# Performance work log

Hardware: AMD Instinct MI355X
Metric: run time of the kernel (lower is better)

The kernel has to match this reference:

```python
import jax, jax.numpy as jnp
import numpy as np

SP = 4      # sp_size (number of simulated sequence-parallel ranks)
NH = 16     # num_attention_heads
HD = 64     # head_dim
HS = 1024   # hidden_size
B = 1       # batch
S = 8192    # global sequence length (SP chunks of 2048)


def setup_inputs() -> dict:
    key = jax.random.key(0)
    ks = jax.random.split(key, 9)
    w_scale = 1.0 / np.sqrt(HS)
    def w(k):
        # xavier-ish init, stored as [in, out] so y = x @ W + b
        return jax.random.uniform(k, (HS, HS), jnp.float32, -w_scale, w_scale)
    return {
        'hidden_states': jax.random.normal(ks[0], (B, S, HS), jnp.float32),
        'Wq': w(ks[1]), 'bq': jnp.zeros((HS,), jnp.float32),
        'Wk': w(ks[2]), 'bk': jnp.zeros((HS,), jnp.float32),
        'Wv': w(ks[3]), 'bv': jnp.zeros((HS,), jnp.float32),
        'Wo': w(ks[4]), 'bo': jnp.zeros((HS,), jnp.float32),
    }


def reference(hidden_states, Wq, bq, Wk, bk, Wv, bv, Wo, bo):
    b, s, _ = hidden_states.shape
    sc = s // SP  # per-rank chunk length
    inv_sqrt_hd = 1.0 / np.sqrt(HD)

    def heads(x):
        # [B, S, HS] -> [SP, B, NH, Sc, HD]
        return x.reshape(b, SP, sc, NH, HD).transpose(1, 0, 3, 2, 4)

    q = heads(hidden_states @ Wq + bq)
    k = heads(hidden_states @ Wk + bk)
    v = heads(hidden_states @ Wv + bv)

    out = jnp.zeros_like(q)
    # ring attention: at step i each rank r attends to chunk (r + i) mod SP
    for i in range(SP):
        ki = jnp.roll(k, -i, axis=0)
        vi = jnp.roll(v, -i, axis=0)
        scores = jnp.einsum('sbhqd,sbhkd->sbhqk', q, ki) * inv_sqrt_hd
        probs = jax.nn.softmax(scores, axis=-1)  # per-chunk softmax (faithful to source)
        out = out + jnp.einsum('sbhqk,sbhkd->sbhqd', probs, vi)
    out = out / SP  # source divides accumulated context by sp_size

    # [SP, B, NH, Sc, HD] -> [B, S, NH*HD]
    ctx = out.transpose(1, 0, 3, 2, 4).reshape(b, s, NH * HD)
    return ctx @ Wo + bo
```

## Files before the change

kernel.cpp:

```cpp
#include <hip/hip_runtime.h>

#define DEVINL __device__ __forceinline__

typedef __attribute__((ext_vector_type(8))) short short8;
typedef __attribute__((ext_vector_type(4))) float floatx4;
typedef __attribute__((ext_vector_type(2))) unsigned uintx2;

DEVINL unsigned short f2bf(float f){
  unsigned u = __builtin_bit_cast(unsigned, f);
  u += 0x7FFFu + ((u >> 16) & 1u);
  return (unsigned short)(u >> 16);
}
DEVINL unsigned pk2(float a, float b){
  unsigned ua = __builtin_bit_cast(unsigned, a);
  unsigned ub = __builtin_bit_cast(unsigned, b);
  ua += 0x7FFFu + ((ua >> 16) & 1u);
  ub += 0x7FFFu + ((ub >> 16) & 1u);
  return (ua >> 16) | (ub & 0xFFFF0000u);
}
DEVINL unsigned pkfast(float a, float b){
  unsigned ua = __builtin_bit_cast(unsigned, a) + 0x8000u;
  unsigned ub = __builtin_bit_cast(unsigned, b) + 0x8000u;
  return __builtin_amdgcn_perm(ub, ua, 0x07060302u);
}
DEVINL unsigned pkbf(float a, float b){
#if defined(__has_builtin)
#if __has_builtin(__builtin_amdgcn_cvt_pk_bf16_f32)
  typedef __attribute__((ext_vector_type(2))) __bf16 bf16x2_t;
  bf16x2_t r = __builtin_amdgcn_cvt_pk_bf16_f32(a, b);
  return __builtin_bit_cast(unsigned, r);
#else
  return pkfast(a, b);
#endif
#else
  return pkfast(a, b);
#endif
}
DEVINL float bf2f(unsigned short h){
  unsigned u = ((unsigned)h) << 16;
  return __builtin_bit_cast(float, u);
}
DEVINL void gload_lds16(const void* g, void* l){
  __builtin_amdgcn_global_load_lds((const __attribute__((address_space(1))) void*)g,
                                   (__attribute__((address_space(3))) void*)l, 16, 0, 0);
}
DEVINL int perm2(int k){
  return (((k >> 4) & 1) << 5) | (((k >> 2) & 3) << 3) | (((k >> 5) & 1) << 2) | (k & 3);
}

__global__ void k_detect(const unsigned* __restrict__ w, int* __restrict__ flag){
  __shared__ int cnt;
  if (threadIdx.x == 0) cnt = 0;
  __syncthreads();
  int c = 0;
  for (int i = threadIdx.x; i < 1024; i += 256){
    unsigned e = (w[i] >> 7) & 0xFFu;
    c += (e >= 120u && e <= 132u) ? 1 : 0;
  }
  atomicAdd(&cnt, c);
  __syncthreads();
  if (threadIdx.x == 0) *flag = (cnt > 512) ? 1 : 0;
}

__global__ void k_conv_bf16(const void* __restrict__ src, unsigned short* __restrict__ dst,
                            int n, const int* __restrict__ flag){
  int i = (blockIdx.x * 256 + threadIdx.x) * 8;
  if (i >= n) return;
  if (*flag){
    ((uint4*)dst)[i >> 3] = ((const uint4*)src)[i >> 3];
  } else {
    const float* s = (const float*)src;
    short8 v;
    #pragma unroll
    for (int j = 0; j < 8; j++) v[j] = (short)f2bf(s[i + j]);
    *(short8*)(dst + i) = v;
  }
}

__global__ void k_conv_wT4(const void* __restrict__ s0, const void* __restrict__ s1,
                           const void* __restrict__ s2, const void* __restrict__ s3,
                           unsigned short* __restrict__ d0, unsigned short* __restrict__ d1,
                           unsigned short* __restrict__ d2, unsigned short* __restrict__ d3,
                           const int* __restrict__ flag){
  __shared__ float tile[32][33];
  const void* src; unsigned short* dst;
  switch (blockIdx.z){
    case 0: src = s0; dst = d0; break;
    case 1: src = s1; dst = d1; break;
    case 2: src = s2; dst = d2; break;
    default: src = s3; dst = d3; break;
  }
  const int tx = threadIdx.x & 31, ty = threadIdx.x >> 5;
  const int bx = blockIdx.x, by = blockIdx.y;
  const int isbf = *flag;
  #pragma unroll
  for (int r = 0; r < 32; r += 8){
    int k = by*32 + ty + r, n = bx*32 + tx;
    float v = isbf ? bf2f(((const unsigned short*)src)[k*1024 + n])
                   : ((const float*)src)[k*1024 + n];
    tile[ty + r][tx] = v;
  }
  __syncthreads();
  #pragma unroll
  for (int r = 0; r < 32; r += 8){
    int n = bx*32 + ty + r, k = by*32 + tx;
    dst[n*1024 + k] = f2bf(tile[tx][ty + r]);
  }
}

__global__ void k_conv_b4(const void* __restrict__ s0, const void* __restrict__ s1,
                          const void* __restrict__ s2, const void* __restrict__ s3,
                          float* __restrict__ dst, const int* __restrict__ flag){
  int i = blockIdx.x * 256 + threadIdx.x;
  if (i >= 4096) return;
  int z = i >> 10, j = i & 1023;
  const void* s = (z == 0) ? s0 : (z == 1) ? s1 : (z == 2) ? s2 : s3;
  dst[i] = (*flag) ? bf2f(((const unsigned short*)s)[j]) : ((const float*)s)[j];
}

template<int MODE>
__global__ __launch_bounds__(256, 2) void k_gemm(
    const unsigned short* __restrict__ A, const unsigned short* __restrict__ Bt,
    const float* __restrict__ bias, void* __restrict__ C0, void* __restrict__ C1,
    void* __restrict__ C2, const int* __restrict__ flagp, float scale)
{
  const int K = 1024;
  __shared__ __align__(16) unsigned short As[128*32];
  __shared__ __align__(16) unsigned short Bs[128*32];
  const int tid = threadIdx.x;
  const int lane = tid & 63, wave = tid >> 6;
  const int quad = lane >> 4, l15 = lane & 15;
  const int m0 = blockIdx.x * 128, n0 = blockIdx.y * 128;
  const int wm = (wave >> 1) * 64, wn = (wave & 1) * 64;
  const floatx4 fzero = {0.f, 0.f, 0.f, 0.f};
  floatx4 acc[4][4];
  #pragma unroll
  for (int i = 0; i < 4; i++)
    #pragma unroll
    for (int j = 0; j < 4; j++) acc[i][j] = fzero;

  for (int k0 = 0; k0 < K; k0 += 32){
    __syncthreads();
    #pragma unroll
    for (int rep = 0; rep < 2; rep++){
      int idx = tid + rep*256;
      int row = idx >> 2, c = idx & 3;
      gload_lds16(A  + (size_t)(m0 + row)*K + (k0 + c*8), &As[idx*8]);
      gload_lds16(Bt + (size_t)(n0 + row)*K + (k0 + c*8), &Bs[idx*8]);
    }
    asm volatile("s_waitcnt vmcnt(0)" ::: "memory");
    __syncthreads();
    short8 af[4], bf[4];
    #pragma unroll
    for (int i = 0; i < 4; i++) af[i] = *(const short8*)&As[(wm + i*16 + l15)*32 + quad*8];
    #pragma unroll
    for (int j = 0; j < 4; j++) bf[j] = *(const short8*)&Bs[(wn + j*16 + l15)*32 + quad*8];
    #pragma unroll
    for (int i = 0; i < 4; i++)
      #pragma unroll
      for (int j = 0; j < 4; j++)
        acc[i][j] = __builtin_amdgcn_mfma_f32_16x16x32_bf16(af[i], bf[j], acc[i][j], 0, 0, 0);
  }

  float bs[4];
  #pragma unroll
  for (int j = 0; j < 4; j++) bs[j] = bias[n0 + wn + j*16 + l15];
  const int useBf = (MODE == 1) ? *flagp : 1;
  #pragma unroll
  for (int i = 0; i < 4; i++){
    #pragma unroll
    for (int j = 0; j < 4; j++){
      int n = n0 + wn + j*16 + l15;
      #pragma unroll
      for (int r = 0; r < 4; r++){
        int m = m0 + wm + i*16 + quad*4 + r;
        float v = acc[i][j][r] + bs[j];
        if (MODE == 3){
          int sel = n >> 10, nn = n & 1023;
          if (sel == 0){
            int dd = (nn & 63) ^ ((m & 7) << 3);
            ((unsigned short*)C0)[((size_t)(nn >> 6)*8192 + m)*64 + dd] = f2bf(v * scale);
          } else if (sel == 1){
            int dd = (nn & 63) ^ ((m & 7) << 3);
            ((unsigned short*)C1)[((size_t)(nn >> 6)*8192 + m)*64 + dd] = f2bf(v);
          } else {
            int s2 = perm2(m & 63) ^ ((nn & 7) << 3);
            ((unsigned short*)C2)[(size_t)nn*8192 + (m & ~63) + s2] = f2bf(v);
          }
        } else {
          if (useBf) ((unsigned short*)C0)[(size_t)m*1024 + n] = f2bf(v);
          else       ((float*)C0)[(size_t)m*1024 + n] = v;
        }
      }
    }
  }
}

__global__ __launch_bounds__(512, 4) void k_attn(
    const unsigned short* __restrict__ Qg, const unsigned short* __restrict__ Kg,
    const unsigned short* __restrict__ Vg, unsigned short* __restrict__ ctx)
{
  __shared__ __align__(16) unsigned short Qs[256*64];
  __shared__ __align__(16) unsigned short Ks[2][64*64];
  __shared__ __align__(16) unsigned short Vs[2][64*64];
  const int tid = threadIdx.x, lane = tid & 63, wave = tid >> 6;
  const int quad = lane >> 4, l15 = lane & 15;
  const int bid = blockIdx.x;
  const int xcd = bid & 7, slot = bid >> 3;
  const int h = xcd*2 + (slot >> 5);
  const int rem = slot & 31, rchunk = rem >> 3, qt = rem & 7;
  const int sq0 = rchunk*2048 + qt*256;
  const char* Qbase = (const char*)(Qg + (size_t)h*8192*64 + (size_t)sq0*64);
  const char* Kbase = (const char*)(Kg + (size_t)h*8192*64);
  const char* Vbase = (const char*)(Vg + (size_t)h*8192*64);
  const int wq0 = wave * 32;
  const floatx4 fz = {0.f, 0.f, 0.f, 0.f};

  const size_t voff = (size_t)(tid >> 3)*16384 + (size_t)(tid & 7)*16;

  auto stage = [&](int buf, int kvs){
    gload_lds16(Kbase + (size_t)kvs*128 + tid*16, (char*)Ks[buf] + tid*16);
    gload_lds16(Vbase + (size_t)kvs*2 + voff,     (char*)Vs[buf] + tid*16);
  };

  #pragma unroll
  for (int rep = 0; rep < 4; rep++){
    int idx = tid + rep*512;
    gload_lds16(Qbase + idx*16, (char*)Qs + idx*16);
  }
  stage(0, rchunk*2048);
  asm volatile("s_waitcnt vmcnt(0)" ::: "memory");
  __syncthreads();

  short8 qf[2][2];
  #pragma unroll
  for (int mi = 0; mi < 2; mi++)
    #pragma unroll
    for (int ks = 0; ks < 2; ks++){
      int row = wq0 + mi*16 + l15;
      qf[mi][ks] = *(const short8*)&Qs[row*64 + (((ks*4 + quad) ^ (row & 7)))*8];
    }

  short8 ones;
  #pragma unroll
  for (int j = 0; j < 8; j++) ones[j] = (short)0x3F80;

  floatx4 Of[2][4];
  #pragma unroll
  for (int mi = 0; mi < 2; mi++)
    #pragma unroll
    for (int di = 0; di < 4; di++) Of[mi][di] = fz;

  for (int i = 0; i < 4; i++){
    floatx4 Oc[2][4], Ol[2];
    #pragma unroll
    for (int mi = 0; mi < 2; mi++){
      Ol[mi] = fz;
      #pragma unroll
      for (int di = 0; di < 4; di++) Oc[mi][di] = fz;
    }

    for (int kt = 0; kt < 32; kt++){
      const int t = i*32 + kt, cur = t & 1;
      asm volatile("s_waitcnt vmcnt(0)" ::: "memory");
      __syncthreads();
      if (t < 127){
        int t1 = t + 1;
        int kvs = ((rchunk + (t1 >> 5)) & 3)*2048 + (t1 & 31)*64;
        stage(cur ^ 1, kvs);
      }

      short8 pf[2][2];
      #pragma unroll
      for (int mi = 0; mi < 2; mi++){
        floatx4 St[4];
        #pragma unroll
        for (int ni = 0; ni < 4; ni++){
          int krow = ni*16 + l15;
          short8 kf = *(const short8*)&Ks[cur][krow*64 + ((quad ^ (krow & 7)))*8];
          St[ni] = __builtin_amdgcn_mfma_f32_16x16x32_bf16(kf, qf[mi][0], fz, 0, 0, 0);
        }
        #pragma unroll
        for (int ni = 0; ni < 4; ni++){
          int krow = ni*16 + l15;
          short8 kf = *(const short8*)&Ks[cur][krow*64 + (((4 + quad) ^ (krow & 7)))*8];
          St[ni] = __builtin_amdgcn_mfma_f32_16x16x32_bf16(kf, qf[mi][1], St[ni], 0, 0, 0);
        }
        #pragma unroll
        for (int ni = 0; ni < 4; ni++)
          #pragma unroll
          for (int r = 0; r < 4; r++)
            St[ni][r] = __builtin_amdgcn_exp2f(St[ni][r]);
        #pragma unroll
        for (int ks = 0; ks < 2; ks++){
          uintx2 lo, hi;
          lo[0] = pkbf(St[ks  ][0], St[ks  ][1]);
          lo[1] = pkbf(St[ks  ][2], St[ks  ][3]);
          hi[0] = pkbf(St[2+ks][0], St[2+ks][1]);
          hi[1] = pkbf(St[2+ks][2], St[2+ks][3]);
          union { uintx2 u[2]; short8 s; } cv;
          cv.u[0] = lo; cv.u[1] = hi;
          pf[mi][ks] = cv.s;
        }
      }

      #pragma unroll
      for (int ks = 0; ks < 2; ks++){
        #pragma unroll
        for (int di = 0; di < 4; di++){
          int vrow = di*16 + l15;
          short8 vf = *(const short8*)&Vs[cur][vrow*64 + (((ks*4 + quad) ^ (vrow & 7)))*8];
          #pragma unroll
          for (int mi = 0; mi < 2; mi++)
            Oc[mi][di] = __builtin_amdgcn_mfma_f32_16x16x32_bf16(vf, pf[mi][ks], Oc[mi][di], 0, 0, 0);
        }
        #pragma unroll
        for (int mi = 0; mi < 2; mi++)
          Ol[mi] = __builtin_amdgcn_mfma_f32_16x16x32_bf16(ones, pf[mi][ks], Ol[mi], 0, 0, 0);
      }
    }

    #pragma unroll
    for (int mi = 0; mi < 2; mi++){
      float inv = __builtin_amdgcn_rcpf(Ol[mi][0]);
      #pragma unroll
      for (int di = 0; di < 4; di++)
        #pragma unroll
        for (int r = 0; r < 4; r++) Of[mi][di][r] += Oc[mi][di][r] * inv;
    }
  }

  #pragma unroll
  for (int mi = 0; mi < 2; mi++){
    int q = sq0 + wq0 + mi*16 + l15;
    #pragma unroll
    for (int di = 0; di < 4; di++){
      uintx2 w;
      w[0] = pk2(Of[mi][di][0]*0.25f, Of[mi][di][1]*0.25f);
      w[1] = pk2(Of[mi][di][2]*0.25f, Of[mi][di][3]*0.25f);
      *(uintx2*)&ctx[(size_t)q*1024 + h*64 + di*16 + quad*4] = w;
    }
  }
}

extern "C" void kernel_launch(void* const* d_in, const int* in_sizes, int n_in,
                              void* d_out, int out_size, void* d_ws, size_t ws_size,
                              hipStream_t stream)
{
  (void)in_sizes; (void)n_in; (void)out_size; (void)ws_size;
  char* ws = (char*)d_ws;
  size_t off = 0;
  auto alloc = [&](size_t bytes) -> char* {
    char* p = ws + off;
    off = (off + bytes + 255) & ~(size_t)255;
    return p;
  };
  int* flag            = (int*)alloc(4);
  unsigned short* hsb  = (unsigned short*)alloc((size_t)8192*1024*2);
  unsigned short* wqt  = (unsigned short*)alloc((size_t)1024*1024*2);
  unsigned short* wkt  = (unsigned short*)alloc((size_t)1024*1024*2);
  unsigned short* wvt  = (unsigned short*)alloc((size_t)1024*1024*2);
  unsigned short* wot  = (unsigned short*)alloc((size_t)1024*1024*2);
  float* biasAll       = (float*)alloc(4096*4);
  unsigned short* Qb   = (unsigned short*)alloc((size_t)16*8192*64*2);
  unsigned short* Kb   = (unsigned short*)alloc((size_t)16*8192*64*2);
  unsigned short* Vb   = (unsigned short*)alloc((size_t)16*8192*64*2);
  unsigned short* ctxb = (unsigned short*)alloc((size_t)8192*1024*2);

  k_detect<<<1, 256, 0, stream>>>((const unsigned*)d_in[0], flag);
  k_conv_bf16<<<4096, 256, 0, stream>>>(d_in[0], hsb, 8192*1024, flag);
  k_conv_wT4<<<dim3(32,32,4), 256, 0, stream>>>(d_in[1], d_in[3], d_in[5], d_in[7],
                                                wqt, wkt, wvt, wot, flag);
  k_conv_b4<<<16, 256, 0, stream>>>(d_in[2], d_in[4], d_in[6], d_in[8], biasAll, flag);

  const float Cs = 0.18033688011112042f;
  k_gemm<3><<<dim3(64, 24), 256, 0, stream>>>(hsb, wqt, biasAll, Qb, Kb, Vb, nullptr, Cs);

  k_attn<<<512, 512, 0, stream>>>(Qb, Kb, Vb, ctxb);

  k_gemm<1><<<dim3(64, 8), 256, 0, stream>>>(ctxb, wot, biasAll + 3072, d_out,
                                             nullptr, nullptr, flag, 1.0f);
}
```

Baseline: 513.5 us.

## Split attention over ring steps into separate blocks with partial-sum reduction

The attention kernel now launches four times as many blocks, each handling a single ring step (one KV chunk) instead of looping over all four. Each block writes its normalized fp32 partial into its own plane, and a new reduction kernel sums the four planes and converts to bf16. If the workspace is too small, it falls back to atomic adds into a zeroed fp32 buffer. The aim is more parallelism and better occupancy across the GPU, at the cost of extra fp32 traffic (four 32 MB planes) and an additional kernel launch.

```diff
diff --git a/kernel.cpp b/kernel.cpp
--- a/kernel.cpp
+++ b/kernel.cpp
@@ -196,9 +196,10 @@
   }
 }
 
+template<int ATOMIC>
 __global__ __launch_bounds__(512, 4) void k_attn(
     const unsigned short* __restrict__ Qg, const unsigned short* __restrict__ Kg,
-    const unsigned short* __restrict__ Vg, unsigned short* __restrict__ ctx)
+    const unsigned short* __restrict__ Vg, float* __restrict__ outp)
 {
   __shared__ __align__(16) unsigned short Qs[256*64];
   __shared__ __align__(16) unsigned short Ks[2][64*64];
@@ -207,9 +208,12 @@
   const int quad = lane >> 4, l15 = lane & 15;
   const int bid = blockIdx.x;
   const int xcd = bid & 7, slot = bid >> 3;
-  const int h = xcd*2 + (slot >> 5);
-  const int rem = slot & 31, rchunk = rem >> 3, qt = rem & 7;
+  const int h = xcd*2 + (slot >> 7);
+  const int rem = slot & 127;
+  const int rchunk = rem >> 5, rem2 = rem & 31;
+  const int cidx = rem2 >> 3, qt = rem2 & 7;
   const int sq0 = rchunk*2048 + qt*256;
+  const int kb = ((rchunk + cidx) & 3)*2048;
   const char* Qbase = (const char*)(Qg + (size_t)h*8192*64 + (size_t)sq0*64);
   const char* Kbase = (const char*)(Kg + (size_t)h*8192*64);
   const char* Vbase = (const char*)(Vg + (size_t)h*8192*64);
@@ -217,7 +221,6 @@
   const floatx4 fz = {0.f, 0.f, 0.f, 0.f};
 
   const size_t voff = (size_t)(tid >> 3)*16384 + (size_t)(tid & 7)*16;
-
   auto stage = [&](int buf, int kvs){
     gload_lds16(Kbase + (size_t)kvs*128 + tid*16, (char*)Ks[buf] + tid*16);
     gload_lds16(Vbase + (size_t)kvs*2 + voff,     (char*)Vs[buf] + tid*16);
@@ -228,7 +231,7 @@
     int idx = tid + rep*512;
     gload_lds16(Qbase + idx*16, (char*)Qs + idx*16);
   }
-  stage(0, rchunk*2048);
+  stage(0, kb);
   asm volatile("s_waitcnt vmcnt(0)" ::: "memory");
   __syncthreads();
 
@@ -245,109 +248,128 @@
   #pragma unroll
   for (int j = 0; j < 8; j++) ones[j] = (short)0x3F80;
 
-  floatx4 Of[2][4];
-  #pragma unroll
-  for (int mi = 0; mi < 2; mi++)
-    #pragma unroll
-    for (int di = 0; di < 4; di++) Of[mi][di] = fz;
-
-  for (int i = 0; i < 4; i++){
-    floatx4 Oc[2][4], Ol[2];
+  floatx4 Oc[2][4], Ol[2];
+  #pragma unroll
+  for (int mi = 0; mi < 2; mi++){
+    Ol[mi] = fz;
+    #pragma unroll
+    for (int di = 0; di < 4; di++) Oc[mi][di] = fz;
+  }
+
+  for (int kt = 0; kt < 32; kt++){
+    const int cur = kt & 1;
+    asm volatile("s_waitcnt vmcnt(0)" ::: "memory");
+    __syncthreads();
+    if (kt < 31) stage(cur ^ 1, kb + (kt + 1)*64);
+
+    short8 pf[2][2];
     #pragma unroll
     for (int mi = 0; mi < 2; mi++){
-      Ol[mi] = fz;
-      #pragma unroll
-      for (int di = 0; di < 4; di++) Oc[mi][di] = fz;
-    }
-
-    for (int kt = 0; kt < 32; kt++){
-      const int t = i*32 + kt, cur = t & 1;
-      asm volatile("s_waitcnt vmcnt(0)" ::: "memory");
-      __syncthreads();
-      if (t < 127){
-        int t1 = t + 1;
-        int kvs = ((rchunk + (t1 >> 5)) & 3)*2048 + (t1 & 31)*64;
-        stage(cur ^ 1, kvs);
-      }
-
-      short8 pf[2][2];
-      #pragma unroll
-      for (int mi = 0; mi < 2; mi++){
-        floatx4 St[4];
+      floatx4 St[4];
+      #pragma unroll
+      for (int ni = 0; ni < 4; ni++){
+        int krow = ni*16 + l15;
+        short8 kf = *(const short8*)&Ks[cur][krow*64 + ((quad ^ (krow & 7)))*8];
+        St[ni] = __builtin_amdgcn_mfma_f32_16x16x32_bf16(kf, qf[mi][0], fz, 0, 0, 0);
+      }
+      #pragma unroll
+      for (int ni = 0; ni < 4; ni++){
+        int krow = ni*16 + l15;
+        short8 kf = *(const short8*)&Ks[cur][krow*64 + (((4 + quad) ^ (krow & 7)))*8];
+        St[ni] = __builtin_amdgcn_mfma_f32_16x16x32_bf16(kf, qf[mi][1], St[ni], 0, 0, 0);
+      }
+      #pragma unroll
+      for (int ni = 0; ni < 4; ni++)
         #pragma unroll
-        for (int ni = 0; ni < 4; ni++){
-          int krow = ni*16 + l15;
-          short8 kf = *(const short8*)&Ks[cur][krow*64 + ((quad ^ (krow & 7)))*8];
-          St[ni] = __builtin_amdgcn_mfma_f32_16x16x32_bf16(kf, qf[mi][0], fz, 0, 0, 0);
-        }
-        #pragma unroll
-        for (int ni = 0; ni < 4; ni++){
-          int krow = ni*16 + l15;
-          short8 kf = *(const short8*)&Ks[cur][krow*64 + (((4 + quad) ^ (krow & 7)))*8];
-          St[ni] = __builtin_amdgcn_mfma_f32_16x16x32_bf16(kf, qf[mi][1], St[ni], 0, 0, 0);
-        }
-        #pragma unroll
-        for (int ni = 0; ni < 4; ni++)
-          #pragma unroll
-          for (int r = 0; r < 4; r++)
-            St[ni][r] = __builtin_amdgcn_exp2f(St[ni][r]);
-        #pragma unroll
-        for (int ks = 0; ks < 2; ks++){
-          uintx2 lo, hi;
-          lo[0] = pkbf(St[ks  ][0], St[ks  ][1]);
-          lo[1] = pkbf(St[ks  ][2], St[ks  ][3]);
-          hi[0] = pkbf(St[2+ks][0], St[2+ks][1]);
-          hi[1] = pkbf(St[2+ks][2], St[2+ks][3]);
-          union { uintx2 u[2]; short8 s; } cv;
-          cv.u[0] = lo; cv.u[1] = hi;
-          pf[mi][ks] = cv.s;
-        }
-      }
-
+        for (int r = 0; r < 4; r++)
+          St[ni][r] = __builtin_amdgcn_exp2f(St[ni][r]);
       #pragma unroll
       for (int ks = 0; ks < 2; ks++){
-        #pragma unroll
-        for (int di = 0; di < 4; di++){
-          int vrow = di*16 + l15;
-          short8 vf = *(const short8*)&Vs[cur][vrow*64 + (((ks*4 + quad) ^ (vrow & 7)))*8];
-          #pragma unroll
-          for (int mi = 0; mi < 2; mi++)
-            Oc[mi][di] = __builtin_amdgcn_mfma_f32_16x16x32_bf16(vf, pf[mi][ks], Oc[mi][di], 0, 0, 0);
-        }
+        uintx2 lo, hi;
+        lo[0] = pkbf(St[ks  ][0], St[ks  ][1]);
+        lo[1] = pkbf(St[ks  ][2], St[ks  ][3]);
+        hi[0] = pkbf(St[2+ks][0], St[2+ks][1]);
+        hi[1] = pkbf(St[2+ks][2], St[2+ks][3]);
+        union { uintx2 u[2]; short8 s; } cv;
+        cv.u[0] = lo; cv.u[1] = hi;
+        pf[mi][ks] = cv.s;
+      }
+    }
+
+    #pragma unroll
+    for (int ks = 0; ks < 2; ks++){
+      #pragma unroll
+      for (int di = 0; di < 4; di++){
+        int vrow = di*16 + l15;
+        short8 vf = *(const short8*)&Vs[cur][vrow*64 + (((ks*4 + quad) ^ (vrow & 7)))*8];
         #pragma unroll
         for (int mi = 0; mi < 2; mi++)
-          Ol[mi] = __builtin_amdgcn_mfma_f32_16x16x32_bf16(ones, pf[mi][ks], Ol[mi], 0, 0, 0);
-      }
-    }
-
-    #pragma unroll
-    for (int mi = 0; mi < 2; mi++){
-      float inv = __builtin_amdgcn_rcpf(Ol[mi][0]);
-      #pragma unroll
-      for (int di = 0; di < 4; di++)
+          Oc[mi][di] = __builtin_amdgcn_mfma_f32_16x16x32_bf16(vf, pf[mi][ks], Oc[mi][di], 0, 0, 0);
+      }
+      #pragma unroll
+      for (int mi = 0; mi < 2; mi++)
+        Ol[mi] = __builtin_amdgcn_mfma_f32_16x16x32_bf16(ones, pf[mi][ks], Ol[mi], 0, 0, 0);
+    }
+  }
+
+  #pragma unroll
+  for (int mi = 0; mi < 2; mi++){
+    float inv = __builtin_amdgcn_rcpf(Ol[mi][0]) * 0.25f;
+    int q = sq0 + wq0 + mi*16 + l15;
+    #pragma unroll
+    for (int di = 0; di < 4; di++){
+      size_t addr = (size_t)q*1024 + h*64 + di*16 + quad*4;
+      if (ATOMIC){
         #pragma unroll
-        for (int r = 0; r < 4; r++) Of[mi][di][r] += Oc[mi][di][r] * inv;
-    }
-  }
-
-  #pragma unroll
-  for (int mi = 0; mi < 2; mi++){
-    int q = sq0 + wq0 + mi*16 + l15;
-    #pragma unroll
-    for (int di = 0; di < 4; di++){
-      uintx2 w;
-      w[0] = pk2(Of[mi][di][0]*0.25f, Of[mi][di][1]*0.25f);
-      w[1] = pk2(Of[mi][di][2]*0.25f, Of[mi][di][3]*0.25f);
-      *(uintx2*)&ctx[(size_t)q*1024 + h*64 + di*16 + quad*4] = w;
-    }
-  }
+        for (int r = 0; r < 4; r++) atomicAdd(&outp[addr + r], Oc[mi][di][r] * inv);
+      } else {
+        floatx4 v;
+        #pragma unroll
+        for (int r = 0; r < 4; r++) v[r] = Oc[mi][di][r] * inv;
+        *(floatx4*)&outp[(size_t)cidx*8192*1024 + addr] = v;
+      }
+    }
+  }
+}
+
+__global__ void k_redux4(const float* __restrict__ part, unsigned short* __restrict__ ctx){
+  const size_t P = (size_t)8192*1024;
+  size_t i = ((size_t)blockIdx.x * 256 + threadIdx.x) * 4;
+  if (i >= P) return;
+  floatx4 a = *(const floatx4*)&part[i];
+  floatx4 b = *(const floatx4*)&part[P + i];
+  floatx4 c = *(const floatx4*)&part[2*P + i];
+  floatx4 d = *(const floatx4*)&part[3*P + i];
+  uintx2 w;
+  w[0] = pk2(a[0]+b[0]+c[0]+d[0], a[1]+b[1]+c[1]+d[1]);
+  w[1] = pk2(a[2]+b[2]+c[2]+d[2], a[3]+b[3]+c[3]+d[3]);
+  *(uintx2*)&ctx[i] = w;
+}
+
+__global__ void k_cvt1(const float* __restrict__ acc, unsigned short* __restrict__ ctx){
+  const size_t P = (size_t)8192*1024;
+  size_t i = ((size_t)blockIdx.x * 256 + threadIdx.x) * 4;
+  if (i >= P) return;
+  floatx4 a = *(const floatx4*)&acc[i];
+  uintx2 w;
+  w[0] = pk2(a[0], a[1]);
+  w[1] = pk2(a[2], a[3]);
+  *(uintx2*)&ctx[i] = w;
+}
+
+__global__ void k_zero(float* __restrict__ p){
+  const size_t P = (size_t)8192*1024;
+  size_t i = ((size_t)blockIdx.x * 256 + threadIdx.x) * 4;
+  if (i >= P) return;
+  floatx4 z = {0.f, 0.f, 0.f, 0.f};
+  *(floatx4*)&p[i] = z;
 }
 
 extern "C" void kernel_launch(void* const* d_in, const int* in_sizes, int n_in,
                               void* d_out, int out_size, void* d_ws, size_t ws_size,
                               hipStream_t stream)
 {
-  (void)in_sizes; (void)n_in; (void)out_size; (void)ws_size;
+  (void)in_sizes; (void)n_in; (void)out_size;
   char* ws = (char*)d_ws;
   size_t off = 0;
   auto alloc = [&](size_t bytes) -> char* {
@@ -356,16 +378,19 @@
     return p;
   };
   int* flag            = (int*)alloc(4);
-  unsigned short* hsb  = (unsigned short*)alloc((size_t)8192*1024*2);
+  float* biasAll       = (float*)alloc(4096*4);
   unsigned short* wqt  = (unsigned short*)alloc((size_t)1024*1024*2);
   unsigned short* wkt  = (unsigned short*)alloc((size_t)1024*1024*2);
   unsigned short* wvt  = (unsigned short*)alloc((size_t)1024*1024*2);
   unsigned short* wot  = (unsigned short*)alloc((size_t)1024*1024*2);
-  float* biasAll       = (float*)alloc(4096*4);
+  unsigned short* hsb  = (unsigned short*)alloc((size_t)8192*1024*2);
   unsigned short* Qb   = (unsigned short*)alloc((size_t)16*8192*64*2);
   unsigned short* Kb   = (unsigned short*)alloc((size_t)16*8192*64*2);
   unsigned short* Vb   = (unsigned short*)alloc((size_t)16*8192*64*2);
-  unsigned short* ctxb = (unsigned short*)alloc((size_t)8192*1024*2);
+  unsigned short* ctxb = hsb;
+  size_t base = off;
+  const size_t PLANE = (size_t)8192*1024*4;
+  const bool planes_fit = (ws_size >= base + 4*PLANE);
 
   k_detect<<<1, 256, 0, stream>>>((const unsigned*)d_in[0], flag);
   k_conv_bf16<<<4096, 256, 0, stream>>>(d_in[0], hsb, 8192*1024, flag);
@@ -376,7 +401,16 @@
   const float Cs = 0.18033688011112042f;
   k_gemm<3><<<dim3(64, 24), 256, 0, stream>>>(hsb, wqt, biasAll, Qb, Kb, Vb, nullptr, Cs);
 
-  k_attn<<<512, 512, 0, stream>>>(Qb, Kb, Vb, ctxb);
+  if (planes_fit){
+    float* part = (float*)(ws + base);
+    k_attn<0><<<2048, 512, 0, stream>>>(Qb, Kb, Vb, part);
+    k_redux4<<<8192, 256, 0, stream>>>(part, ctxb);
+  } else {
+    float* ctxf = (float*)(ws + base);
+    k_zero<<<8192, 256, 0, stream>>>(ctxf);
+    k_attn<1><<<2048, 512, 0, stream>>>(Qb, Kb, Vb, ctxf);
+    k_cvt1<<<8192, 256, 0, stream>>>(ctxf, ctxb);
+  }
 
   k_gemm<1><<<dim3(64, 8), 256, 0, stream>>>(ctxb, wot, biasAll + 3072, d_out,
                                              nullptr, nullptr, flag, 1.0f);
```

Result: faster. 487.7 us (-5.0%).
